# Performance work log

Hardware: AMD Instinct MI355X
Metric: run time of the kernel (lower is better)

The kernel has to match this reference:

```python
import jax, jax.numpy as jnp
import numpy as np

B, N_NUM, F_CAT, N_CAT = 262144, 64, 32, 8
N_FEATURE = N_NUM + F_CAT * N_CAT  # 320
N_PHENOTYPE = N_NUM + F_CAT        # 96


def setup_inputs() -> dict:
    key = jax.random.key(0)
    k1, k2, k3, k4 = jax.random.split(key, 4)
    return {
        "numerical_x": jax.random.normal(k1, (B, N_NUM), dtype=jnp.float32),
        "categorical_x": jax.random.uniform(k2, (F_CAT, B, N_CAT), dtype=jnp.float32),
        "W": jax.random.normal(k3, (2, N_FEATURE), dtype=jnp.float32),
        "M": jax.random.normal(k4, (2, N_PHENOTYPE), dtype=jnp.float32),
    }


def reference(numerical_x, categorical_x, W, M):
    # numerical_x: [B, n_num]; categorical_x: [F, B, n_cat]; W: [2, n_feature]; M: [2, n_phenotype]
    b, n_num = numerical_x.shape
    f_cat, _, n_cat = categorical_x.shape
    W_num = W[:, :n_num]                           # [2, n_num], one column per numerical feature
    W_cat = W[:, n_num:].reshape(2, f_cat, n_cat)  # contiguous slices k:k+n per categorical feature
    # numerical: W[:,[k]] @ x.mT is an outer product of W column k with the k-th feature column
    t_num = jnp.tanh(W_num[:, :, None] * numerical_x.T[None, :, :])   # [2, n_num, B]
    s_num = jnp.sum(t_num * M[:, :n_num, None], axis=1)               # [2, B]
    # categorical: W[:,k:k+n] @ x.mT for each feature block, batched over features
    t_cat = jnp.tanh(jnp.einsum('cfn,fbn->cfb', W_cat, categorical_x))  # [2, F, B]
    s_cat = jnp.sum(t_cat * M[:, n_num:, None], axis=1)               # [2, B]
    f = s_num + s_cat                                                 # [2, B]
    ef = jnp.exp(f)
    return ef / jnp.sum(ef, axis=0, keepdims=True)                    # prob over the 2-class axis
```

## Files before the change

kernel.cpp:

```cpp
#include <hip/hip_runtime.h>

constexpr int Bn    = 262144;
constexpr int NNUM  = 64;
constexpr int FCAT  = 32;
constexpr int NCAT  = 8;
constexpr int NFEAT = NNUM + FCAT * NCAT;
constexpr int NPHEN = NNUM + FCAT;

__device__ __forceinline__ float tanh_from_2x(float a) {
    float e = __expf(a);
    float r = __builtin_amdgcn_rcpf(e + 1.0f);
    return fmaf(-2.0f, r, 1.0f);
}

__global__ __launch_bounds__(256) void model_kernel(
    const float* __restrict__ num_x,
    const float* __restrict__ cat_x,
    const float* __restrict__ W,
    const float* __restrict__ M,
    float* __restrict__ out)
{
    __shared__ float sW2[2 * NFEAT];
    __shared__ float sM[2 * NPHEN];
    const int tid = threadIdx.x;
    for (int i = tid; i < 2 * NFEAT; i += 256) sW2[i] = 2.0f * W[i];
    for (int i = tid; i < 2 * NPHEN; i += 256) sM[i] = M[i];
    __syncthreads();

    const int b = blockIdx.x * 256 + tid;

    float f0 = 0.0f, f1 = 0.0f;

    const float4* nx = reinterpret_cast<const float4*>(num_x + (size_t)b * NNUM);
    #pragma unroll
    for (int i = 0; i < NNUM / 4; ++i) {
        float4 v = nx[i];
        const float* vp = reinterpret_cast<const float*>(&v);
        #pragma unroll
        for (int j = 0; j < 4; ++j) {
            const int k = i * 4 + j;
            float x  = vp[j];
            float t0 = tanh_from_2x(sW2[k] * x);
            float t1 = tanh_from_2x(sW2[NFEAT + k] * x);
            f0 = fmaf(sM[k], t0, f0);
            f1 = fmaf(sM[NPHEN + k], t1, f1);
        }
    }

    #pragma unroll 4
    for (int f = 0; f < FCAT; ++f) {
        const float4* cx = reinterpret_cast<const float4*>(
            cat_x + (size_t)f * (size_t)Bn * NCAT + (size_t)b * NCAT);
        float4 v0 = cx[0];
        float4 v1 = cx[1];
        const float* vp0 = reinterpret_cast<const float*>(&v0);
        const float* vp1 = reinterpret_cast<const float*>(&v1);
        const float* w0 = &sW2[NNUM + f * NCAT];
        const float* w1 = &sW2[NFEAT + NNUM + f * NCAT];
        float d0 = 0.0f, d1 = 0.0f;
        #pragma unroll
        for (int n = 0; n < 4; ++n) {
            d0 = fmaf(w0[n], vp0[n], d0);
            d1 = fmaf(w1[n], vp0[n], d1);
        }
        #pragma unroll
        for (int n = 0; n < 4; ++n) {
            d0 = fmaf(w0[4 + n], vp1[n], d0);
            d1 = fmaf(w1[4 + n], vp1[n], d1);
        }
        float t0 = tanh_from_2x(d0);
        float t1 = tanh_from_2x(d1);
        f0 = fmaf(sM[NNUM + f], t0, f0);
        f1 = fmaf(sM[NPHEN + NNUM + f], t1, f1);
    }

    float e10 = __expf(f1 - f0);
    float o0  = __builtin_amdgcn_rcpf(1.0f + e10);
    out[b]             = o0;
    out[(size_t)Bn + b] = 1.0f - o0;
}

extern "C" void kernel_launch(void* const* d_in, const int* in_sizes, int n_in,
                              void* d_out, int out_size, void* d_ws, size_t ws_size,
                              hipStream_t stream) {
    const float* num_x = (const float*)d_in[0];
    const float* cat_x = (const float*)d_in[1];
    const float* W     = (const float*)d_in[2];
    const float* M     = (const float*)d_in[3];
    float* out = (float*)d_out;

    dim3 grid(Bn / 256), block(256);
    hipLaunchKernelGGL(model_kernel, grid, block, 0, stream,
                       num_x, cat_x, W, M, out);
}
```

Baseline: 67.79 us.

## Prescale weights in a prep kernel and read them as uniform scalar loads

A small prep kernel now scales W by 2*log2(e) into workspace once per call. The main kernel drops its per-block shared-memory staging and barrier, reading weights and M directly from global memory as wave-uniform loads, and uses exp2 instead of expf inside tanh. The categorical loop is fully unrolled. The aim is to remove the per-block LDS fill, the __syncthreads and LDS read traffic, and to save a multiply per exp. In exchange it adds a second kernel launch and leans on scalar or cached loads for the weights.

```diff
diff --git a/kernel.cpp b/kernel.cpp
--- a/kernel.cpp
+++ b/kernel.cpp
@@ -7,8 +7,17 @@
 constexpr int NFEAT = NNUM + FCAT * NCAT;
 constexpr int NPHEN = NNUM + FCAT;
 
-__device__ __forceinline__ float tanh_from_2x(float a) {
-    float e = __expf(a);
+constexpr float TWO_LOG2E = 2.8853900817779268f;
+
+__global__ __launch_bounds__(256) void prep_kernel(
+    const float* __restrict__ W, float* __restrict__ Wp)
+{
+    int i = blockIdx.x * 256 + threadIdx.x;
+    if (i < 2 * NFEAT) Wp[i] = TWO_LOG2E * W[i];
+}
+
+__device__ __forceinline__ float tanh_e2(float a) {
+    float e = __builtin_amdgcn_exp2f(a);
     float r = __builtin_amdgcn_rcpf(e + 1.0f);
     return fmaf(-2.0f, r, 1.0f);
 }
@@ -16,18 +25,11 @@
 __global__ __launch_bounds__(256) void model_kernel(
     const float* __restrict__ num_x,
     const float* __restrict__ cat_x,
-    const float* __restrict__ W,
+    const float* __restrict__ Wp,
     const float* __restrict__ M,
     float* __restrict__ out)
 {
-    __shared__ float sW2[2 * NFEAT];
-    __shared__ float sM[2 * NPHEN];
-    const int tid = threadIdx.x;
-    for (int i = tid; i < 2 * NFEAT; i += 256) sW2[i] = 2.0f * W[i];
-    for (int i = tid; i < 2 * NPHEN; i += 256) sM[i] = M[i];
-    __syncthreads();
-
-    const int b = blockIdx.x * 256 + tid;
+    const int b = blockIdx.x * 256 + threadIdx.x;
 
     float f0 = 0.0f, f1 = 0.0f;
 
@@ -39,44 +41,38 @@
         #pragma unroll
         for (int j = 0; j < 4; ++j) {
             const int k = i * 4 + j;
-            float x  = vp[j];
-            float t0 = tanh_from_2x(sW2[k] * x);
-            float t1 = tanh_from_2x(sW2[NFEAT + k] * x);
-            f0 = fmaf(sM[k], t0, f0);
-            f1 = fmaf(sM[NPHEN + k], t1, f1);
+            float x = vp[j];
+            f0 = fmaf(M[k],         tanh_e2(Wp[k] * x),         f0);
+            f1 = fmaf(M[NPHEN + k], tanh_e2(Wp[NFEAT + k] * x), f1);
         }
     }
 
-    #pragma unroll 4
+    #pragma unroll
     for (int f = 0; f < FCAT; ++f) {
         const float4* cx = reinterpret_cast<const float4*>(
             cat_x + (size_t)f * (size_t)Bn * NCAT + (size_t)b * NCAT);
         float4 v0 = cx[0];
         float4 v1 = cx[1];
-        const float* vp0 = reinterpret_cast<const float*>(&v0);
-        const float* vp1 = reinterpret_cast<const float*>(&v1);
-        const float* w0 = &sW2[NNUM + f * NCAT];
-        const float* w1 = &sW2[NFEAT + NNUM + f * NCAT];
+        const float* p0 = reinterpret_cast<const float*>(&v0);
+        const float* p1 = reinterpret_cast<const float*>(&v1);
         float d0 = 0.0f, d1 = 0.0f;
         #pragma unroll
         for (int n = 0; n < 4; ++n) {
-            d0 = fmaf(w0[n], vp0[n], d0);
-            d1 = fmaf(w1[n], vp0[n], d1);
+            d0 = fmaf(Wp[NNUM + f * NCAT + n],         p0[n], d0);
+            d1 = fmaf(Wp[NFEAT + NNUM + f * NCAT + n], p0[n], d1);
         }
         #pragma unroll
         for (int n = 0; n < 4; ++n) {
-            d0 = fmaf(w0[4 + n], vp1[n], d0);
-            d1 = fmaf(w1[4 + n], vp1[n], d1);
+            d0 = fmaf(Wp[NNUM + f * NCAT + 4 + n],         p1[n], d0);
+            d1 = fmaf(Wp[NFEAT + NNUM + f * NCAT + 4 + n], p1[n], d1);
         }
-        float t0 = tanh_from_2x(d0);
-        float t1 = tanh_from_2x(d1);
-        f0 = fmaf(sM[NNUM + f], t0, f0);
-        f1 = fmaf(sM[NPHEN + NNUM + f], t1, f1);
+        f0 = fmaf(M[NNUM + f],         tanh_e2(d0), f0);
+        f1 = fmaf(M[NPHEN + NNUM + f], tanh_e2(d1), f1);
     }
 
     float e10 = __expf(f1 - f0);
     float o0  = __builtin_amdgcn_rcpf(1.0f + e10);
-    out[b]             = o0;
+    out[b]              = o0;
     out[(size_t)Bn + b] = 1.0f - o0;
 }
 
@@ -88,8 +84,9 @@
     const float* W     = (const float*)d_in[2];
     const float* M     = (const float*)d_in[3];
     float* out = (float*)d_out;
+    float* Wp  = (float*)d_ws;
 
-    dim3 grid(Bn / 256), block(256);
-    hipLaunchKernelGGL(model_kernel, grid, block, 0, stream,
-                       num_x, cat_x, W, M, out);
+    hipLaunchKernelGGL(prep_kernel, dim3(3), dim3(256), 0, stream, W, Wp);
+    hipLaunchKernelGGL(model_kernel, dim3(Bn / 256), dim3(256), 0, stream,
+                       num_x, cat_x, Wp, M, out);
 }
```

Measured after the change: 74.45 us. +9.8%, slower.

## Double-buffer categorical loads in registers and use nontemporal loads/stores

Applied to the files above, without the earlier changes.

The first batch of categorical-feature loads is issued before the shared-memory barrier, and the categorical loop becomes a register double-buffered pipeline that prefetches the next four features while computing the current four. All global loads and stores switch to nontemporal hints. The intent is to hide memory latency in a bandwidth-bound streaming kernel. The cost is higher register pressure (16 float4 buffers), which may reduce occupancy.

```diff
diff --git a/kernel.cpp b/kernel.cpp
--- a/kernel.cpp
+++ b/kernel.cpp
@@ -6,6 +6,8 @@
 constexpr int NCAT  = 8;
 constexpr int NFEAT = NNUM + FCAT * NCAT;
 constexpr int NPHEN = NNUM + FCAT;
+
+typedef float fx4 __attribute__((ext_vector_type(4)));
 
 __device__ __forceinline__ float tanh_from_2x(float a) {
     float e = __expf(a);
@@ -25,59 +27,76 @@
     const int tid = threadIdx.x;
     for (int i = tid; i < 2 * NFEAT; i += 256) sW2[i] = 2.0f * W[i];
     for (int i = tid; i < 2 * NPHEN; i += 256) sM[i] = M[i];
-    __syncthreads();
 
     const int b = blockIdx.x * 256 + tid;
+    const float* cbase = cat_x + (size_t)b * NCAT;
+    const size_t fstride = (size_t)Bn * NCAT;
+
+    fx4 bufA[8], bufB[8];
+    #pragma unroll
+    for (int q = 0; q < 4; ++q) {
+        const fx4* cx = reinterpret_cast<const fx4*>(cbase + (size_t)q * fstride);
+        bufA[q * 2 + 0] = __builtin_nontemporal_load(cx);
+        bufA[q * 2 + 1] = __builtin_nontemporal_load(cx + 1);
+    }
+
+    __syncthreads();
 
     float f0 = 0.0f, f1 = 0.0f;
 
-    const float4* nx = reinterpret_cast<const float4*>(num_x + (size_t)b * NNUM);
+    const fx4* nx = reinterpret_cast<const fx4*>(num_x + (size_t)b * NNUM);
     #pragma unroll
     for (int i = 0; i < NNUM / 4; ++i) {
-        float4 v = nx[i];
-        const float* vp = reinterpret_cast<const float*>(&v);
+        fx4 v = __builtin_nontemporal_load(nx + i);
         #pragma unroll
         for (int j = 0; j < 4; ++j) {
             const int k = i * 4 + j;
-            float x  = vp[j];
-            float t0 = tanh_from_2x(sW2[k] * x);
-            float t1 = tanh_from_2x(sW2[NFEAT + k] * x);
-            f0 = fmaf(sM[k], t0, f0);
-            f1 = fmaf(sM[NPHEN + k], t1, f1);
+            float x  = v[j];
+            f0 = fmaf(sM[k],         tanh_from_2x(sW2[k] * x),         f0);
+            f1 = fmaf(sM[NPHEN + k], tanh_from_2x(sW2[NFEAT + k] * x), f1);
         }
     }
 
-    #pragma unroll 4
-    for (int f = 0; f < FCAT; ++f) {
-        const float4* cx = reinterpret_cast<const float4*>(
-            cat_x + (size_t)f * (size_t)Bn * NCAT + (size_t)b * NCAT);
-        float4 v0 = cx[0];
-        float4 v1 = cx[1];
-        const float* vp0 = reinterpret_cast<const float*>(&v0);
-        const float* vp1 = reinterpret_cast<const float*>(&v1);
-        const float* w0 = &sW2[NNUM + f * NCAT];
-        const float* w1 = &sW2[NFEAT + NNUM + f * NCAT];
-        float d0 = 0.0f, d1 = 0.0f;
-        #pragma unroll
-        for (int n = 0; n < 4; ++n) {
-            d0 = fmaf(w0[n], vp0[n], d0);
-            d1 = fmaf(w1[n], vp0[n], d1);
+    #pragma unroll
+    for (int g = 0; g < 8; ++g) {
+        fx4* cur = (g & 1) ? bufB : bufA;
+        fx4* nxt = (g & 1) ? bufA : bufB;
+        if (g < 7) {
+            #pragma unroll
+            for (int q = 0; q < 4; ++q) {
+                const int f = (g + 1) * 4 + q;
+                const fx4* cx = reinterpret_cast<const fx4*>(cbase + (size_t)f * fstride);
+                nxt[q * 2 + 0] = __builtin_nontemporal_load(cx);
+                nxt[q * 2 + 1] = __builtin_nontemporal_load(cx + 1);
+            }
         }
         #pragma unroll
-        for (int n = 0; n < 4; ++n) {
-            d0 = fmaf(w0[4 + n], vp1[n], d0);
-            d1 = fmaf(w1[4 + n], vp1[n], d1);
+        for (int q = 0; q < 4; ++q) {
+            const int f = g * 4 + q;
+            const fx4 v0 = cur[q * 2 + 0];
+            const fx4 v1 = cur[q * 2 + 1];
+            const float* w0 = &sW2[NNUM + f * NCAT];
+            const float* w1 = &sW2[NFEAT + NNUM + f * NCAT];
+            float d0 = 0.0f, d1 = 0.0f;
+            #pragma unroll
+            for (int n = 0; n < 4; ++n) {
+                d0 = fmaf(w0[n], v0[n], d0);
+                d1 = fmaf(w1[n], v0[n], d1);
+            }
+            #pragma unroll
+            for (int n = 0; n < 4; ++n) {
+                d0 = fmaf(w0[4 + n], v1[n], d0);
+                d1 = fmaf(w1[4 + n], v1[n], d1);
+            }
+            f0 = fmaf(sM[NNUM + f],         tanh_from_2x(d0), f0);
+            f1 = fmaf(sM[NPHEN + NNUM + f], tanh_from_2x(d1), f1);
         }
-        float t0 = tanh_from_2x(d0);
-        float t1 = tanh_from_2x(d1);
-        f0 = fmaf(sM[NNUM + f], t0, f0);
-        f1 = fmaf(sM[NPHEN + NNUM + f], t1, f1);
     }
 
     float e10 = __expf(f1 - f0);
     float o0  = __builtin_amdgcn_rcpf(1.0f + e10);
-    out[b]             = o0;
-    out[(size_t)Bn + b] = 1.0f - o0;
+    __builtin_nontemporal_store(o0,        out + b);
+    __builtin_nontemporal_store(1.0f - o0, out + (size_t)Bn + b);
 }
 
 extern "C" void kernel_launch(void* const* d_in, const int* in_sizes, int n_in,
```

New measurement: 91.47 us. 34.9% more time.

## Split each row's features across two threads and combine with shuffle

Applied to the files above, without the earlier changes.

Each batch row is now handled by two adjacent threads. One takes the first half of the numerical and categorical features, the other takes the second half, and a lane shuffle adds their partial logits. The grid doubles and the launch bounds now ask for more resident waves, which exposes more memory-level parallelism for this bandwidth-bound kernel. In exchange the shared-memory setup of W and M runs in twice as many blocks, and the paired threads now read strided halves of each row, which can hurt coalescing.

```diff
diff --git a/kernel.cpp b/kernel.cpp
--- a/kernel.cpp
+++ b/kernel.cpp
@@ -7,13 +7,15 @@
 constexpr int NFEAT = NNUM + FCAT * NCAT;
 constexpr int NPHEN = NNUM + FCAT;
 
+typedef float fx4 __attribute__((ext_vector_type(4)));
+
 __device__ __forceinline__ float tanh_from_2x(float a) {
     float e = __expf(a);
     float r = __builtin_amdgcn_rcpf(e + 1.0f);
     return fmaf(-2.0f, r, 1.0f);
 }
 
-__global__ __launch_bounds__(256) void model_kernel(
+__global__ __launch_bounds__(256, 8) void model_kernel(
     const float* __restrict__ num_x,
     const float* __restrict__ cat_x,
     const float* __restrict__ W,
@@ -27,57 +29,58 @@
     for (int i = tid; i < 2 * NPHEN; i += 256) sM[i] = M[i];
     __syncthreads();
 
-    const int b = blockIdx.x * 256 + tid;
+    const int gt = blockIdx.x * 256 + tid;
+    const int b  = gt >> 1;
+    const int p  = gt & 1;
 
     float f0 = 0.0f, f1 = 0.0f;
 
-    const float4* nx = reinterpret_cast<const float4*>(num_x + (size_t)b * NNUM);
+    const int k0 = p * 32;
+    const fx4* nx = reinterpret_cast<const fx4*>(num_x + (size_t)b * NNUM + k0);
     #pragma unroll
-    for (int i = 0; i < NNUM / 4; ++i) {
-        float4 v = nx[i];
-        const float* vp = reinterpret_cast<const float*>(&v);
+    for (int i = 0; i < 8; ++i) {
+        fx4 v = nx[i];
         #pragma unroll
         for (int j = 0; j < 4; ++j) {
-            const int k = i * 4 + j;
-            float x  = vp[j];
-            float t0 = tanh_from_2x(sW2[k] * x);
-            float t1 = tanh_from_2x(sW2[NFEAT + k] * x);
-            f0 = fmaf(sM[k], t0, f0);
-            f1 = fmaf(sM[NPHEN + k], t1, f1);
+            const int k = k0 + i * 4 + j;
+            float x = v[j];
+            f0 = fmaf(sM[k],         tanh_from_2x(sW2[k] * x),         f0);
+            f1 = fmaf(sM[NPHEN + k], tanh_from_2x(sW2[NFEAT + k] * x), f1);
         }
     }
 
+    const int fbase = p * 16;
     #pragma unroll 4
-    for (int f = 0; f < FCAT; ++f) {
-        const float4* cx = reinterpret_cast<const float4*>(
+    for (int fi = 0; fi < 16; ++fi) {
+        const int f = fbase + fi;
+        const fx4* cx = reinterpret_cast<const fx4*>(
             cat_x + (size_t)f * (size_t)Bn * NCAT + (size_t)b * NCAT);
-        float4 v0 = cx[0];
-        float4 v1 = cx[1];
-        const float* vp0 = reinterpret_cast<const float*>(&v0);
-        const float* vp1 = reinterpret_cast<const float*>(&v1);
+        fx4 v0 = cx[0];
+        fx4 v1 = cx[1];
         const float* w0 = &sW2[NNUM + f * NCAT];
         const float* w1 = &sW2[NFEAT + NNUM + f * NCAT];
         float d0 = 0.0f, d1 = 0.0f;
         #pragma unroll
         for (int n = 0; n < 4; ++n) {
-            d0 = fmaf(w0[n], vp0[n], d0);
-            d1 = fmaf(w1[n], vp0[n], d1);
+            d0 = fmaf(w0[n], v0[n], d0);
+            d1 = fmaf(w1[n], v0[n], d1);
         }
         #pragma unroll
         for (int n = 0; n < 4; ++n) {
-            d0 = fmaf(w0[4 + n], vp1[n], d0);
-            d1 = fmaf(w1[4 + n], vp1[n], d1);
+            d0 = fmaf(w0[4 + n], v1[n], d0);
+            d1 = fmaf(w1[4 + n], v1[n], d1);
         }
-        float t0 = tanh_from_2x(d0);
-        float t1 = tanh_from_2x(d1);
-        f0 = fmaf(sM[NNUM + f], t0, f0);
-        f1 = fmaf(sM[NPHEN + NNUM + f], t1, f1);
+        f0 = fmaf(sM[NNUM + f],         tanh_from_2x(d0), f0);
+        f1 = fmaf(sM[NPHEN + NNUM + f], tanh_from_2x(d1), f1);
     }
+
+    f0 += __shfl_xor(f0, 1);
+    f1 += __shfl_xor(f1, 1);
 
     float e10 = __expf(f1 - f0);
     float o0  = __builtin_amdgcn_rcpf(1.0f + e10);
-    out[b]             = o0;
-    out[(size_t)Bn + b] = 1.0f - o0;
+    if (p == 0) out[b] = o0;
+    else        out[(size_t)Bn + b] = 1.0f - o0;
 }
 
 extern "C" void kernel_launch(void* const* d_in, const int* in_sizes, int n_in,
@@ -89,7 +92,7 @@
     const float* M     = (const float*)d_in[3];
     float* out = (float*)d_out;
 
-    dim3 grid(Bn / 256), block(256);
+    dim3 grid(2 * Bn / 256), block(256);
     hipLaunchKernelGGL(model_kernel, grid, block, 0, stream,
                        num_x, cat_x, W, M, out);
 }
```

Result: slower. 69.23 us (+2.1%).
